# Performance work log

Measured on AMD Instinct MI355X. Metric: run time of the kernel, lower is better.

Reference implementation:

```python
import jax, jax.numpy as jnp
import numpy as np

M, NQ, NK, DZ, DX = 8, 1024, 1024, 256, 2
H, HD = 8, 32            # num_heads, head_dim
KH = 32                  # kernel MLP hidden width
INNER = H * HD           # 256


def setup_inputs() -> dict:
    key = jax.random.key(0)
    ks = jax.random.split(key, 12)
    f32 = jnp.float32
    return {
        "zq":  jax.random.normal(ks[0], (M, NQ, DZ), dtype=f32),
        "zk":  jax.random.normal(ks[1], (M, NK, DZ), dtype=f32),
        "zv":  jax.random.normal(ks[2], (M, NK, DZ), dtype=f32),
        "xq":  jax.random.normal(ks[3], (M, NQ, DX), dtype=f32),
        "xkv": jax.random.normal(ks[4], (M, NK, DX), dtype=f32),
        # projection weights (nn.Linear, bias=False); stored [in, out]
        "Wq":  jax.random.normal(ks[5], (DZ, INNER), dtype=f32) * 0.02,
        "Wk":  jax.random.normal(ks[6], (DZ, INNER), dtype=f32) * 0.02,
        "Wv":  jax.random.normal(ks[7], (DZ, INNER), dtype=f32) * 0.02,
        # output projection (Linear with bias; dropout p=0 -> identity)
        "Wout": jax.random.normal(ks[8], (INNER, DZ), dtype=f32) * 0.02,
        "bout": jnp.zeros((DZ,), dtype=f32),
        # kernel MLP: (dx + h) -> KH -> h
        "W1": jax.random.normal(ks[9], (DX + H, KH), dtype=f32) * 0.3,
        "b1": jnp.zeros((KH,), dtype=f32),
        "W2": jax.random.normal(ks[10], (KH, H), dtype=f32) * 0.3,
        "b2": jnp.zeros((H,), dtype=f32),
    }


def reference(zq, zk, zv, xq, xkv, Wq, Wk, Wv, Wout, bout, W1, b1, W2, b2):
    m, nq, _ = zq.shape
    nk = zk.shape[1]
    scale = HD ** -0.5

    # translation group action: pairwise position differences [m,nq,nk,dx]
    diff = xq[:, :, None, :] - xkv[:, None, :, :]

    q = (zq @ Wq).reshape(m, nq, H, HD)
    k = (zk @ Wk).reshape(m, nk, H, HD)
    v = (zv @ Wv).reshape(m, nk, H, HD)

    # token dots, already laid out as [m,nq,nk,h]
    token_dots = jnp.einsum("mqhd,mkhd->mqkh", q, k) * scale

    # kernel MLP over concatenated [diff, token_dots]: [m,nq,nk,dx+h] -> [m,nq,nk,h]
    kernel_input = jnp.concatenate([diff, token_dots], axis=-1)
    dots = jax.nn.relu(kernel_input @ W1 + b1) @ W2 + b2

    # softmax over keys (nk axis)
    attn = jax.nn.softmax(dots, axis=2)  # [m,nq,nk,h]

    out = jnp.einsum("mqkh,mkhd->mqhd", attn, v).reshape(m, nq, INNER)
    out = out @ Wout + bout

    # phi is None -> query locations pass through unchanged
    xq_new = xq
    return out, xq_new
```

## Files before the change

### kernel.cpp

```cpp
#include <hip/hip_runtime.h>

typedef float f32x4 __attribute__((ext_vector_type(4)));
typedef short s16x8 __attribute__((ext_vector_type(8)));
typedef _Float16 h2 __attribute__((ext_vector_type(2)));
typedef unsigned short u16;

using fp16x2 = decltype(__builtin_amdgcn_cvt_pkrtz(0.0f, 0.0f));

#define MFMA16 __builtin_amdgcn_mfma_f32_16x16x32_bf16
#define SCALE 0.17677669529663687f

#if defined(__has_builtin)
#if __has_builtin(__builtin_amdgcn_fdot2)
#define HAS_FDOT2 1
#endif
#endif

__device__ __forceinline__ h2 cvt_pk(float a, float b) {
  return __builtin_bit_cast(h2, __builtin_amdgcn_cvt_pkrtz(a, b));
}

__device__ __forceinline__ float fdot2f(h2 a, h2 b, float c) {
#ifdef HAS_FDOT2
  return __builtin_amdgcn_fdot2(__builtin_bit_cast(fp16x2, a),
                                __builtin_bit_cast(fp16x2, b), c, false);
#else
  return fmaf((float)a.x, (float)b.x, fmaf((float)a.y, (float)b.y, c));
#endif
}

__device__ __forceinline__ u16 f2b(float f) {
  union { float f; unsigned u; } x; x.f = f;
  unsigned r = x.u + 0x7fffu + ((x.u >> 16) & 1u);
  return (u16)(r >> 16);
}
__device__ __forceinline__ float b2f(u16 s) {
  union { unsigned u; float f; } x; x.u = ((unsigned)s) << 16;
  return x.f;
}

__global__ __launch_bounds__(256) void wtrans_kernel(
    const float* __restrict__ Wq, const float* __restrict__ Wk,
    const float* __restrict__ Wv, const float* __restrict__ Wo,
    u16* __restrict__ WqT, u16* __restrict__ WkT,
    u16* __restrict__ WvT, u16* __restrict__ WoT) {
  const float* src; u16* dst;
  switch (blockIdx.x) {
    case 0: src = Wq; dst = WqT; break;
    case 1: src = Wk; dst = WkT; break;
    case 2: src = Wv; dst = WvT; break;
    default: src = Wo; dst = WoT; break;
  }
  int j = blockIdx.y;
  int d = threadIdx.x;
  dst[j * 256 + d] = f2b(src[d * 256 + j]);
}

__global__ __launch_bounds__(256) void copyxq_kernel(const float* __restrict__ xq,
                                                     float* __restrict__ dst) {
  int i = blockIdx.x * 256 + threadIdx.x;
  dst[i] = xq[i];
}

__global__ __launch_bounds__(256) void proj_kernel(
    const float* __restrict__ zq, const float* __restrict__ zk,
    const float* __restrict__ zv,
    const u16* __restrict__ WqT, const u16* __restrict__ WkT,
    const u16* __restrict__ WvT,
    u16* __restrict__ qb, u16* __restrict__ kb, u16* __restrict__ vT) {
  const int mat = blockIdx.z;
  const float* Z = (mat == 0) ? zq : (mat == 1) ? zk : zv;
  const u16* WT = (mat == 0) ? WqT : (mat == 1) ? WkT : WvT;
  const int n0 = blockIdx.x * 64;
  const int j0 = blockIdx.y * 64;
  const int tid = threadIdx.x;
  const int lane = tid & 63, wid = tid >> 6;
  const int l15 = lane & 15, lg = lane >> 4;
  const int wn = wid & 1, wj = wid >> 1;

  __shared__ u16 As[64][40];
  __shared__ u16 Bs[64][40];

  f32x4 acc[2][2];
  #pragma unroll
  for (int a = 0; a < 2; ++a)
    #pragma unroll
    for (int b = 0; b < 2; ++b) acc[a][b] = (f32x4){0.f, 0.f, 0.f, 0.f};

  for (int ks = 0; ks < 8; ++ks) {
    const int d0 = ks * 32;
    const int r = tid >> 2, cb = (tid & 3) * 8;
    const float* zsrc = &Z[(size_t)(n0 + r) * 256 + d0 + cb];
    s16x8 t;
    #pragma unroll
    for (int j = 0; j < 8; ++j) t[j] = (short)f2b(zsrc[j]);
    *(s16x8*)&As[r][cb] = t;
    *(s16x8*)&Bs[r][cb] = *(const s16x8*)&WT[(size_t)(j0 + r) * 256 + d0 + cb];
    __syncthreads();
    s16x8 a0 = *(const s16x8*)&As[wn * 32 + l15][lg * 8];
    s16x8 a1 = *(const s16x8*)&As[wn * 32 + 16 + l15][lg * 8];
    s16x8 b0 = *(const s16x8*)&Bs[wj * 32 + l15][lg * 8];
    s16x8 b1 = *(const s16x8*)&Bs[wj * 32 + 16 + l15][lg * 8];
    acc[0][0] = MFMA16(a0, b0, acc[0][0], 0, 0, 0);
    acc[0][1] = MFMA16(a0, b1, acc[0][1], 0, 0, 0);
    acc[1][0] = MFMA16(a1, b0, acc[1][0], 0, 0, 0);
    acc[1][1] = MFMA16(a1, b1, acc[1][1], 0, 0, 0);
    __syncthreads();
  }
  #pragma unroll
  for (int sn = 0; sn < 2; ++sn)
    #pragma unroll
    for (int sj = 0; sj < 2; ++sj)
      #pragma unroll
      for (int i = 0; i < 4; ++i) {
        int n = n0 + wn * 32 + sn * 16 + lg * 4 + i;
        int j = j0 + wj * 32 + sj * 16 + l15;
        float av = acc[sn][sj][i];
        if (mat == 0) av *= SCALE;
        u16 val = f2b(av);
        if (mat == 0) {
          qb[(size_t)n * 256 + j] = val;
        } else if (mat == 1) {
          kb[(size_t)n * 256 + j] = val;
        } else {
          int mm = n >> 10, nn = n & 1023;
          vT[((size_t)(mm * 256 + j)) * 1024 + nn] = val;
        }
      }
}

__global__ __launch_bounds__(512, 6) void attn_kernel(
    const u16* __restrict__ qb, const u16* __restrict__ kb,
    const u16* __restrict__ vT,
    const float* __restrict__ xq, const float* __restrict__ xkv,
    const float* __restrict__ W1, const float* __restrict__ b1,
    const float* __restrict__ W2, const float* __restrict__ b2,
    u16* __restrict__ preP, float* __restrict__ Lb) {
  const int m = blockIdx.y;
  const int q0 = blockIdx.x * 16;
  const int kz = blockIdx.z;
  const int tid = threadIdx.x;
  const int lane = tid & 63;
  const int wid = tid >> 6;
  const int l15 = lane & 15;
  const int lg = lane >> 4;
  const int kk = wid * 16 + l15;

  u16* myPre = preP + (size_t)kz * (8192 * 256);
  float* myL = Lb + (size_t)kz * (8192 * 8);

  __shared__ u16 q_s[16][264];
  __shared__ u16 P_s[8][16][136];
  __shared__ unsigned Wc[32][16];

  {
    int r = tid >> 5, cb = (tid & 31) * 8;
    *(s16x8*)&q_s[r][cb] = *(const s16x8*)&qb[((size_t)(m * 1024 + q0 + r)) * 256 + cb];
  }
  if (tid < 32) {
    const int c = tid;
    #pragma unroll
    for (int j = 0; j < 5; ++j) {
      h2 p = cvt_pk(W1[(2 * j) * 32 + c], W1[(2 * j + 1) * 32 + c]);
      Wc[c][j] = __builtin_bit_cast(unsigned, p);
    }
    Wc[c][5] = __builtin_bit_cast(unsigned, b1[c]);
    #pragma unroll
    for (int j = 0; j < 4; ++j) {
      h2 p = cvt_pk(W2[c * 8 + 2 * j], W2[c * 8 + 2 * j + 1]);
      Wc[c][8 + j] = __builtin_bit_cast(unsigned, p);
    }
  }

  float xq0[4], xq1[4];
  #pragma unroll
  for (int i = 0; i < 4; ++i) {
    const float2 v = *(const float2*)&xq[((size_t)(m * 1024 + q0 + lg * 4 + i)) * 2];
    xq0[i] = v.x; xq1[i] = v.y;
  }
  h2 b2p[4];
  #pragma unroll
  for (int j = 0; j < 4; ++j) b2p[j] = cvt_pk(b2[2 * j], b2[2 * j + 1]);

  s16x8 ones;
  #pragma unroll
  for (int j = 0; j < 8; ++j) ones[j] = (l15 == 0) ? (short)0x3F80 : (short)0;

  f32x4 acc_pv[2];
  acc_pv[0] = (f32x4){0.f, 0.f, 0.f, 0.f};
  acc_pv[1] = (f32x4){0.f, 0.f, 0.f, 0.f};
  f32x4 acc_sum = (f32x4){0.f, 0.f, 0.f, 0.f};
  const f32x4 Z4 = (f32x4){0.f, 0.f, 0.f, 0.f};

  __syncthreads();

  for (int kt = 0; kt < 2; ++kt) {
    const int kg = kz * 256 + kt * 128;

    f32x4 dacc[8];
    #pragma unroll
    for (int h = 0; h < 8; ++h) {
      const s16x8 a = *(const s16x8*)&q_s[l15][h * 32 + lg * 8];
      const s16x8 b = *(const s16x8*)&kb[((size_t)(m * 1024 + kg + kk)) * 256 + h * 32 + lg * 8];
      dacc[h] = MFMA16(a, b, Z4, 0, 0, 0);
    }
    h2 dpk[4][4];
    #pragma unroll
    for (int hp = 0; hp < 4; ++hp)
      #pragma unroll
      for (int i = 0; i < 4; ++i)
        dpk[hp][i] = cvt_pk(dacc[2 * hp][i], dacc[2 * hp + 1][i]);

    const float2 xk = *(const float2*)&xkv[((size_t)(m * 1024 + kg + kk)) * 2];
    h2 dqpk[4];
    #pragma unroll
    for (int i = 0; i < 4; ++i)
      dqpk[i] = cvt_pk(xq0[i] - xk.x, xq1[i] - xk.y);

    h2 lgp[4][4];
    #pragma unroll
    for (int i = 0; i < 4; ++i)
      #pragma unroll
      for (int j = 0; j < 4; ++j) lgp[i][j] = b2p[j];

    #pragma unroll 2
    for (int c = 0; c < 32; ++c) {
      const uint4 wa = *(const uint4*)&Wc[c][0];
      const uint2 wb = *(const uint2*)&Wc[c][4];
      const uint4 wcc = *(const uint4*)&Wc[c][8];
      const h2 w10 = __builtin_bit_cast(h2, wa.x), w11 = __builtin_bit_cast(h2, wa.y);
      const h2 w12 = __builtin_bit_cast(h2, wa.z), w13 = __builtin_bit_cast(h2, wa.w);
      const h2 w14 = __builtin_bit_cast(h2, wb.x);
      const float b1c = __builtin_bit_cast(float, wb.y);
      const h2 w20 = __builtin_bit_cast(h2, wcc.x), w21 = __builtin_bit_cast(h2, wcc.y);
      const h2 w22 = __builtin_bit_cast(h2, wcc.z), w23 = __builtin_bit_cast(h2, wcc.w);
      #pragma unroll
      for (int i = 0; i < 4; ++i) {
        float s = fdot2f(dqpk[i], w10, b1c);
        s = fdot2f(dpk[0][i], w11, s);
        s = fdot2f(dpk[1][i], w12, s);
        s = fdot2f(dpk[2][i], w13, s);
        s = fdot2f(dpk[3][i], w14, s);
        const float hv = fmaxf(s, 0.0f);
        const h2 hh = cvt_pk(hv, hv);
        lgp[i][0] += hh * w20;
        lgp[i][1] += hh * w21;
        lgp[i][2] += hh * w22;
        lgp[i][3] += hh * w23;
      }
    }

    #pragma unroll
    for (int i = 0; i < 4; ++i) {
      const int qr = lg * 4 + i;
      #pragma unroll
      for (int j = 0; j < 4; ++j) {
        const float e0 = __expf((float)lgp[i][j].x);
        const float e1 = __expf((float)lgp[i][j].y);
        P_s[2 * j][qr][kk] = (u16)(__builtin_bit_cast(unsigned, e0) >> 16);
        P_s[2 * j + 1][qr][kk] = (u16)(__builtin_bit_cast(unsigned, e1) >> 16);
      }
    }
    __syncthreads();

    s16x8 pa[4];
    #pragma unroll
    for (int ks = 0; ks < 4; ++ks)
      pa[ks] = *(const s16x8*)&P_s[wid][l15][ks * 32 + lg * 8];
    #pragma unroll
    for (int dh = 0; dh < 2; ++dh) {
      const size_t vrow = ((size_t)(m * 256 + wid * 32 + dh * 16 + l15)) * 1024 + kg;
      #pragma unroll
      for (int ks = 0; ks < 4; ++ks) {
        const s16x8 b = *(const s16x8*)&vT[vrow + ks * 32 + lg * 8];
        acc_pv[dh] = MFMA16(pa[ks], b, acc_pv[dh], 0, 0, 0);
      }
    }
    #pragma unroll
    for (int ks = 0; ks < 4; ++ks)
      acc_sum = MFMA16(pa[ks], ones, acc_sum, 0, 0, 0);
    __syncthreads();
  }

  #pragma unroll
  for (int dh = 0; dh < 2; ++dh)
    #pragma unroll
    for (int i = 0; i < 4; ++i) {
      const int qr = lg * 4 + i;
      myPre[((size_t)(m * 1024 + q0 + qr)) * 256 + wid * 32 + dh * 16 + l15] = f2b(acc_pv[dh][i]);
    }
  if (l15 == 0) {
    #pragma unroll
    for (int i = 0; i < 4; ++i)
      myL[((size_t)(m * 1024 + q0 + lg * 4 + i)) * 8 + wid] = acc_sum[i];
  }
}

__global__ __launch_bounds__(256) void outp_kernel(
    const u16* __restrict__ preP, const float* __restrict__ Lb,
    const u16* __restrict__ WoT,
    const float* __restrict__ bout, float* __restrict__ out) {
  const int n0 = blockIdx.x * 64;
  const int j0 = blockIdx.y * 64;
  const int tid = threadIdx.x;
  const int lane = tid & 63, wid = tid >> 6;
  const int l15 = lane & 15, lg = lane >> 4;
  const int wn = wid & 1, wj = wid >> 1;
  __shared__ u16 As[64][40];
  __shared__ u16 Bs[64][40];
  f32x4 acc[2][2];
  #pragma unroll
  for (int a = 0; a < 2; ++a)
    #pragma unroll
    for (int b = 0; b < 2; ++b) acc[a][b] = (f32x4){0.f, 0.f, 0.f, 0.f};

  const size_t PSTRIDE = (size_t)8192 * 256;
  const size_t LSTRIDE = (size_t)8192 * 8;

  for (int ks = 0; ks < 8; ++ks) {
    const int d0 = ks * 32;
    const int r = tid >> 2, cb = (tid & 3) * 8;
    const size_t row = (size_t)(n0 + r);
    const float Ls = Lb[row * 8 + ks] + Lb[LSTRIDE + row * 8 + ks] +
                     Lb[2 * LSTRIDE + row * 8 + ks] + Lb[3 * LSTRIDE + row * 8 + ks];
    const float inv = 1.0f / Ls;
    const s16x8 p0 = *(const s16x8*)&preP[row * 256 + d0 + cb];
    const s16x8 p1 = *(const s16x8*)&preP[PSTRIDE + row * 256 + d0 + cb];
    const s16x8 p2 = *(const s16x8*)&preP[2 * PSTRIDE + row * 256 + d0 + cb];
    const s16x8 p3 = *(const s16x8*)&preP[3 * PSTRIDE + row * 256 + d0 + cb];
    s16x8 t;
    #pragma unroll
    for (int j = 0; j < 8; ++j) {
      const float v = (b2f((u16)p0[j]) + b2f((u16)p1[j]) + b2f((u16)p2[j]) + b2f((u16)p3[j])) * inv;
      t[j] = (short)f2b(v);
    }
    *(s16x8*)&As[r][cb] = t;
    *(s16x8*)&Bs[r][cb] = *(const s16x8*)&WoT[(size_t)(j0 + r) * 256 + d0 + cb];
    __syncthreads();
    s16x8 a0 = *(const s16x8*)&As[wn * 32 + l15][lg * 8];
    s16x8 a1 = *(const s16x8*)&As[wn * 32 + 16 + l15][lg * 8];
    s16x8 b0 = *(const s16x8*)&Bs[wj * 32 + l15][lg * 8];
    s16x8 b1 = *(const s16x8*)&Bs[wj * 32 + 16 + l15][lg * 8];
    acc[0][0] = MFMA16(a0, b0, acc[0][0], 0, 0, 0);
    acc[0][1] = MFMA16(a0, b1, acc[0][1], 0, 0, 0);
    acc[1][0] = MFMA16(a1, b0, acc[1][0], 0, 0, 0);
    acc[1][1] = MFMA16(a1, b1, acc[1][1], 0, 0, 0);
    __syncthreads();
  }
  #pragma unroll
  for (int sn = 0; sn < 2; ++sn)
    #pragma unroll
    for (int sj = 0; sj < 2; ++sj)
      #pragma unroll
      for (int i = 0; i < 4; ++i) {
        int n = n0 + wn * 32 + sn * 16 + lg * 4 + i;
        int j = j0 + wj * 32 + sj * 16 + l15;
        out[(size_t)n * 256 + j] = acc[sn][sj][i] + bout[j];
      }
}

extern "C" void kernel_launch(void* const* d_in, const int* in_sizes, int n_in,
                              void* d_out, int out_size, void* d_ws, size_t ws_size,
                              hipStream_t stream) {
  const float* zq = (const float*)d_in[0];
  const float* zk = (const float*)d_in[1];
  const float* zv = (const float*)d_in[2];
  const float* xq = (const float*)d_in[3];
  const float* xkv = (const float*)d_in[4];
  const float* Wq = (const float*)d_in[5];
  const float* Wk = (const float*)d_in[6];
  const float* Wv = (const float*)d_in[7];
  const float* Wo = (const float*)d_in[8];
  const float* bout = (const float*)d_in[9];
  const float* W1 = (const float*)d_in[10];
  const float* b1 = (const float*)d_in[11];
  const float* W2 = (const float*)d_in[12];
  const float* b2 = (const float*)d_in[13];
  float* out = (float*)d_out;

  const size_t MB = (size_t)1 << 20;
  char* ws = (char*)d_ws;
  u16* qb   = (u16*)(ws + 0 * MB);
  u16* kb   = (u16*)(ws + 4 * MB);
  u16* vT   = (u16*)(ws + 8 * MB);
  u16* preP = (u16*)(ws + 12 * MB);
  float* Lb = (float*)(ws + 28 * MB);
  u16* WqT  = (u16*)(ws + 29 * MB + 0 * (128 << 10));
  u16* WkT  = (u16*)(ws + 29 * MB + 1 * (128 << 10));
  u16* WvT  = (u16*)(ws + 29 * MB + 2 * (128 << 10));
  u16* WoT  = (u16*)(ws + 29 * MB + 3 * (128 << 10));

  wtrans_kernel<<<dim3(4, 256), dim3(256), 0, stream>>>(Wq, Wk, Wv, Wo, WqT, WkT, WvT, WoT);
  proj_kernel<<<dim3(128, 4, 3), dim3(256), 0, stream>>>(zq, zk, zv, WqT, WkT, WvT, qb, kb, vT);
  attn_kernel<<<dim3(64, 8, 4), dim3(512), 0, stream>>>(qb, kb, vT, xq, xkv, W1, b1, W2, b2, preP, Lb);
  outp_kernel<<<dim3(128, 4), dim3(256), 0, stream>>>(preP, Lb, WoT, bout, out);
  copyxq_kernel<<<dim3(64), dim3(256), 0, stream>>>(xq, out + (size_t)8 * 1024 * 256);
}
```

Before: 149.4 us.

## Run kernel MLP layers on bf16 MFMA instead of packed fp16 dot loops

The per-pair kernel MLP (10->32 ReLU ->8) moves from scalar fdot2/packed-half FMA loops onto 16x16x32 bf16 MFMA instructions. Token dots and position differences are packed into bf16 operands through LDS scratch buffers, with b1 folded in as a ones column. Q is now read straight from global memory rather than staged in LDS, and the occupancy hint drops from 6 to 4. This trades VALU work for MFMA work, extra LDS round trips and bf16 precision for the MLP, and lower occupancy.

```diff
diff --git a/kernel.cpp b/kernel.cpp
--- a/kernel.cpp
+++ b/kernel.cpp
@@ -2,32 +2,11 @@
 
 typedef float f32x4 __attribute__((ext_vector_type(4)));
 typedef short s16x8 __attribute__((ext_vector_type(8)));
-typedef _Float16 h2 __attribute__((ext_vector_type(2)));
 typedef unsigned short u16;
-
-using fp16x2 = decltype(__builtin_amdgcn_cvt_pkrtz(0.0f, 0.0f));
+typedef unsigned int u32;
 
 #define MFMA16 __builtin_amdgcn_mfma_f32_16x16x32_bf16
 #define SCALE 0.17677669529663687f
-
-#if defined(__has_builtin)
-#if __has_builtin(__builtin_amdgcn_fdot2)
-#define HAS_FDOT2 1
-#endif
-#endif
-
-__device__ __forceinline__ h2 cvt_pk(float a, float b) {
-  return __builtin_bit_cast(h2, __builtin_amdgcn_cvt_pkrtz(a, b));
-}
-
-__device__ __forceinline__ float fdot2f(h2 a, h2 b, float c) {
-#ifdef HAS_FDOT2
-  return __builtin_amdgcn_fdot2(__builtin_bit_cast(fp16x2, a),
-                                __builtin_bit_cast(fp16x2, b), c, false);
-#else
-  return fmaf((float)a.x, (float)b.x, fmaf((float)a.y, (float)b.y, c));
-#endif
-}
 
 __device__ __forceinline__ u16 f2b(float f) {
   union { float f; unsigned u; } x; x.f = f;
@@ -37,6 +16,16 @@
 __device__ __forceinline__ float b2f(u16 s) {
   union { unsigned u; float f; } x; x.u = ((unsigned)s) << 16;
   return x.f;
+}
+__device__ __forceinline__ u32 pk2(float a, float b) {
+  u32 ua = (__builtin_bit_cast(u32, a) + 0x8000u) >> 16;
+  u32 ub = (__builtin_bit_cast(u32, b) + 0x8000u) & 0xFFFF0000u;
+  return ua | ub;
+}
+__device__ __forceinline__ s16x8 mk8(u32 a, u32 b, u32 c, u32 d) {
+  union { u32 w[4]; s16x8 v; } u;
+  u.w[0] = a; u.w[1] = b; u.w[2] = c; u.w[3] = d;
+  return u.v;
 }
 
 __global__ __launch_bounds__(256) void wtrans_kernel(
@@ -129,7 +118,7 @@
       }
 }
 
-__global__ __launch_bounds__(512, 6) void attn_kernel(
+__global__ __launch_bounds__(512, 4) void attn_kernel(
     const u16* __restrict__ qb, const u16* __restrict__ kb,
     const u16* __restrict__ vT,
     const float* __restrict__ xq, const float* __restrict__ xkv,
@@ -149,38 +138,35 @@
   u16* myPre = preP + (size_t)kz * (8192 * 256);
   float* myL = Lb + (size_t)kz * (8192 * 8);
 
-  __shared__ u16 q_s[16][264];
+  __shared__ u32 IN2[8][16][68];
+  __shared__ u32 H_s[8][16][20];
   __shared__ u16 P_s[8][16][136];
-  __shared__ unsigned Wc[32][16];
-
-  {
-    int r = tid >> 5, cb = (tid & 31) * 8;
-    *(s16x8*)&q_s[r][cb] = *(const s16x8*)&qb[((size_t)(m * 1024 + q0 + r)) * 256 + cb];
-  }
-  if (tid < 32) {
-    const int c = tid;
-    #pragma unroll
-    for (int j = 0; j < 5; ++j) {
-      h2 p = cvt_pk(W1[(2 * j) * 32 + c], W1[(2 * j + 1) * 32 + c]);
-      Wc[c][j] = __builtin_bit_cast(unsigned, p);
-    }
-    Wc[c][5] = __builtin_bit_cast(unsigned, b1[c]);
-    #pragma unroll
-    for (int j = 0; j < 4; ++j) {
-      h2 p = cvt_pk(W2[c * 8 + 2 * j], W2[c * 8 + 2 * j + 1]);
-      Wc[c][8 + j] = __builtin_bit_cast(unsigned, p);
-    }
-  }
-
-  float xq0[4], xq1[4];
-  #pragma unroll
-  for (int i = 0; i < 4; ++i) {
-    const float2 v = *(const float2*)&xq[((size_t)(m * 1024 + q0 + lg * 4 + i)) * 2];
-    xq0[i] = v.x; xq1[i] = v.y;
-  }
-  h2 b2p[4];
-  #pragma unroll
-  for (int j = 0; j < 4; ++j) b2p[j] = cvt_pk(b2[2 * j], b2[2 * j + 1]);
+
+  s16x8 w1a[2];
+  #pragma unroll
+  for (int cblk = 0; cblk < 2; ++cblk) {
+    const int c = cblk * 16 + l15;
+    #pragma unroll
+    for (int j = 0; j < 8; ++j) {
+      const int dim = lg * 8 + j;
+      u16 v = 0;
+      if (dim < 10) v = f2b(W1[dim * 32 + c]);
+      else if (dim == 10) v = f2b(b1[c]);
+      w1a[cblk][j] = (short)v;
+    }
+  }
+  s16x8 w2a;
+  #pragma unroll
+  for (int j = 0; j < 8; ++j) {
+    const int c = lg * 8 + j;
+    w2a[j] = (short)((l15 < 8) ? f2b(W2[c * 8 + l15]) : (u16)0);
+  }
+  float b2r[4];
+  #pragma unroll
+  for (int i = 0; i < 4; ++i) b2r[i] = b2[(lg & 1) * 4 + i];
+
+  const u32 u1base = (lg == 1) ? 0x00003F80u : 0u;
+  const bool lglo = (lg < 2);
 
   s16x8 ones;
   #pragma unroll
@@ -192,73 +178,57 @@
   f32x4 acc_sum = (f32x4){0.f, 0.f, 0.f, 0.f};
   const f32x4 Z4 = (f32x4){0.f, 0.f, 0.f, 0.f};
 
-  __syncthreads();
-
   for (int kt = 0; kt < 2; ++kt) {
     const int kg = kz * 256 + kt * 128;
-
-    f32x4 dacc[8];
-    #pragma unroll
-    for (int h = 0; h < 8; ++h) {
-      const s16x8 a = *(const s16x8*)&q_s[l15][h * 32 + lg * 8];
-      const s16x8 b = *(const s16x8*)&kb[((size_t)(m * 1024 + kg + kk)) * 256 + h * 32 + lg * 8];
-      dacc[h] = MFMA16(a, b, Z4, 0, 0, 0);
-    }
-    h2 dpk[4][4];
-    #pragma unroll
-    for (int hp = 0; hp < 4; ++hp)
-      #pragma unroll
-      for (int i = 0; i < 4; ++i)
-        dpk[hp][i] = cvt_pk(dacc[2 * hp][i], dacc[2 * hp + 1][i]);
-
-    const float2 xk = *(const float2*)&xkv[((size_t)(m * 1024 + kg + kk)) * 2];
-    h2 dqpk[4];
-    #pragma unroll
-    for (int i = 0; i < 4; ++i)
-      dqpk[i] = cvt_pk(xq0[i] - xk.x, xq1[i] - xk.y);
-
-    h2 lgp[4][4];
-    #pragma unroll
-    for (int i = 0; i < 4; ++i)
-      #pragma unroll
-      for (int j = 0; j < 4; ++j) lgp[i][j] = b2p[j];
-
-    #pragma unroll 2
-    for (int c = 0; c < 32; ++c) {
-      const uint4 wa = *(const uint4*)&Wc[c][0];
-      const uint2 wb = *(const uint2*)&Wc[c][4];
-      const uint4 wcc = *(const uint4*)&Wc[c][8];
-      const h2 w10 = __builtin_bit_cast(h2, wa.x), w11 = __builtin_bit_cast(h2, wa.y);
-      const h2 w12 = __builtin_bit_cast(h2, wa.z), w13 = __builtin_bit_cast(h2, wa.w);
-      const h2 w14 = __builtin_bit_cast(h2, wb.x);
-      const float b1c = __builtin_bit_cast(float, wb.y);
-      const h2 w20 = __builtin_bit_cast(h2, wcc.x), w21 = __builtin_bit_cast(h2, wcc.y);
-      const h2 w22 = __builtin_bit_cast(h2, wcc.z), w23 = __builtin_bit_cast(h2, wcc.w);
+    const float2 xk2 = *(const float2*)&xkv[((size_t)(m * 1024 + kg + kk)) * 2];
+
+    {
+      f32x4 dacc[8];
+      #pragma unroll
+      for (int h = 0; h < 8; ++h) {
+        const s16x8 a = *(const s16x8*)&qb[((size_t)(m * 1024 + q0 + l15)) * 256 + h * 32 + lg * 8];
+        const s16x8 b = *(const s16x8*)&kb[((size_t)(m * 1024 + kg + kk)) * 256 + h * 32 + lg * 8];
+        dacc[h] = MFMA16(a, b, Z4, 0, 0, 0);
+      }
       #pragma unroll
       for (int i = 0; i < 4; ++i) {
-        float s = fdot2f(dqpk[i], w10, b1c);
-        s = fdot2f(dpk[0][i], w11, s);
-        s = fdot2f(dpk[1][i], w12, s);
-        s = fdot2f(dpk[2][i], w13, s);
-        s = fdot2f(dpk[3][i], w14, s);
-        const float hv = fmaxf(s, 0.0f);
-        const h2 hh = cvt_pk(hv, hv);
-        lgp[i][0] += hh * w20;
-        lgp[i][1] += hh * w21;
-        lgp[i][2] += hh * w22;
-        lgp[i][3] += hh * w23;
-      }
-    }
-
-    #pragma unroll
-    for (int i = 0; i < 4; ++i) {
-      const int qr = lg * 4 + i;
-      #pragma unroll
-      for (int j = 0; j < 4; ++j) {
-        const float e0 = __expf((float)lgp[i][j].x);
-        const float e1 = __expf((float)lgp[i][j].y);
-        P_s[2 * j][qr][kk] = (u16)(__builtin_bit_cast(unsigned, e0) >> 16);
-        P_s[2 * j + 1][qr][kk] = (u16)(__builtin_bit_cast(unsigned, e1) >> 16);
+        uint4 w;
+        w.x = pk2(dacc[0][i], dacc[1][i]);
+        w.y = pk2(dacc[2][i], dacc[3][i]);
+        w.z = pk2(dacc[4][i], dacc[5][i]);
+        w.w = pk2(dacc[6][i], dacc[7][i]);
+        *(uint4*)&IN2[wid][l15][(lg * 4 + i) * 4] = w;
+      }
+    }
+
+    #pragma unroll 4
+    for (int qg = 0; qg < 16; ++qg) {
+      const uint4 p = *(const uint4*)&IN2[wid][l15][qg * 4];
+      const float2 xq2 = *(const float2*)&xq[((size_t)(m * 1024 + q0 + qg)) * 2];
+      const u32 dqpair = pk2(xq2.x - xk2.x, xq2.y - xk2.y);
+      const u32 u0 = (lg == 0) ? dqpair : ((lg == 1) ? p.w : 0u);
+      const u32 u1 = (lg == 0) ? p.x : u1base;
+      const u32 u2 = (lg == 0) ? p.y : 0u;
+      const u32 u3 = (lg == 0) ? p.z : 0u;
+      const s16x8 bf1 = mk8(u0, u1, u2, u3);
+      const f32x4 h0 = MFMA16(w1a[0], bf1, Z4, 0, 0, 0);
+      const f32x4 h1 = MFMA16(w1a[1], bf1, Z4, 0, 0, 0);
+      uint2 ha, hb;
+      ha.x = pk2(fmaxf(h0[0], 0.f), fmaxf(h0[1], 0.f));
+      ha.y = pk2(fmaxf(h0[2], 0.f), fmaxf(h0[3], 0.f));
+      hb.x = pk2(fmaxf(h1[0], 0.f), fmaxf(h1[1], 0.f));
+      hb.y = pk2(fmaxf(h1[2], 0.f), fmaxf(h1[3], 0.f));
+      *(uint2*)&H_s[wid][l15][2 * lg] = ha;
+      *(uint2*)&H_s[wid][l15][8 + 2 * lg] = hb;
+      const uint4 hv = *(const uint4*)&H_s[wid][l15][lg * 4];
+      const s16x8 bf2 = mk8(hv.x, hv.y, hv.z, hv.w);
+      const f32x4 Lg = MFMA16(w2a, bf2, Z4, 0, 0, 0);
+      if (lglo) {
+        #pragma unroll
+        for (int i = 0; i < 4; ++i) {
+          const float e = __expf(Lg[i] + b2r[i]);
+          P_s[lg * 4 + i][qg][kk] = (u16)(__builtin_bit_cast(unsigned, e) >> 16);
+        }
       }
     }
     __syncthreads();
```

Result: slower. 160.4 us (+7.4%).
